# Performance work log

Measured on AMD Instinct MI355X. Metric: run time of the kernel, lower is better.

## Reference

```python
import jax, jax.numpy as jnp
import numpy as np

N_HEAD = 16
MASK_NEG = -10000.0


def setup_inputs() -> dict:
    key = jax.random.key(0)
    k1, k2, k3 = jax.random.split(key, 3)
    B, S, D = 4, 2048, 1024
    x = jax.random.normal(k1, (B, S, D), dtype=jnp.float32)
    c_attn_w = jax.random.normal(k2, (D, 3 * D), dtype=jnp.float32) * 0.02
    c_attn_b = jnp.zeros((3 * D,), dtype=jnp.float32)
    c_proj_w = jax.random.normal(k3, (D, D), dtype=jnp.float32) * 0.02
    c_proj_b = jnp.zeros((D,), dtype=jnp.float32)
    return {"x": x, "c_attn_w": c_attn_w, "c_attn_b": c_attn_b,
            "c_proj_w": c_proj_w, "c_proj_b": c_proj_b}


def reference(x, c_attn_w, c_attn_b, c_proj_w, c_proj_b):
    B, S, D = x.shape
    H = N_HEAD
    Dh = D // H
    # fused QKV projection (Conv1D = x @ W + b)
    qkv = x @ c_attn_w + c_attn_b          # [B,S,3D]
    q, k, v = jnp.split(qkv, 3, axis=-1)   # each [B,S,D]
    # split heads -> [B,H,S,Dh]
    q = q.reshape(B, S, H, Dh).transpose(0, 2, 1, 3)
    k = k.reshape(B, S, H, Dh).transpose(0, 2, 1, 3)
    v = v.reshape(B, S, H, Dh).transpose(0, 2, 1, 3)
    # scores with scaling (scale=True)
    w = jnp.einsum('bhqd,bhkd->bhqk', q, k) / jnp.sqrt(jnp.float32(Dh))
    # multiplicative causal mask: w*b + -10000*(1-b)
    b = jnp.tril(jnp.ones((S, S), dtype=w.dtype))[None, None]  # [1,1,S,S]
    w = w * b + MASK_NEG * (1.0 - b)
    w = jax.nn.softmax(w, axis=-1)
    # dropout is identity at inference
    a = jnp.einsum('bhqk,bhkd->bhqd', w, v)  # [B,H,S,Dh]
    a = a.transpose(0, 2, 1, 3).reshape(B, S, D)  # merge heads
    out = a @ c_proj_w + c_proj_b
    return out
```

## Files before the change

kernel.cpp:

```cpp
#include <hip/hip_runtime.h>

typedef unsigned short u16;
typedef short bf16x8 __attribute__((ext_vector_type(8)));
typedef float f32x4 __attribute__((ext_vector_type(4)));
typedef unsigned int u32;
typedef u32 u32x4 __attribute__((ext_vector_type(4)));

#define B_ 4
#define S_ 2048
#define D_ 1024
#define H_ 16
#define DH_ 64
#define M_ 8192
#define SCL2E 0.1803368801111244f

__device__ __forceinline__ u16 f2b(float f) {
  union { float f; unsigned int u; } v; v.f = f;
  unsigned int u = v.u;
  unsigned int r = (u + 0x7FFFu + ((u >> 16) & 1u)) >> 16;
  return (u16)r;
}

__device__ __forceinline__ void gload16(const void* g, void* l) {
  __builtin_amdgcn_global_load_lds(
      (const __attribute__((address_space(1))) unsigned int*)g,
      (__attribute__((address_space(3))) unsigned int*)l,
      16, 0, 0);
}

__device__ __forceinline__ u32 cvt_pk_bf16(float lo, float hi) {
  u32 r;
  asm("v_cvt_pk_bf16_f32 %0, %1, %2" : "=v"(r) : "v"(lo), "v"(hi));
  return r;
}

struct __attribute__((aligned(8))) u16x4 { u16 x, y, z, w; };

__global__ void cvt_f32_bf16(const float* __restrict__ in, u16* __restrict__ out, int n) {
  int i = (blockIdx.x * blockDim.x + threadIdx.x) * 4;
  if (i >= n) return;
  float4 v = *(const float4*)(in + i);
  u16x4 o; o.x = f2b(v.x); o.y = f2b(v.y); o.z = f2b(v.z); o.w = f2b(v.w);
  *(u16x4*)(out + i) = o;
}

__global__ void transpose_cvt(const float* __restrict__ in, u16* __restrict__ out, int R, int C) {
  __shared__ float tile[32][33];
  int c0 = blockIdx.x * 32, r0 = blockIdx.y * 32;
  int tx = threadIdx.x, ty = threadIdx.y;
#pragma unroll
  for (int j = 0; j < 32; j += 8)
    tile[ty + j][tx] = in[(size_t)(r0 + ty + j) * C + c0 + tx];
  __syncthreads();
#pragma unroll
  for (int j = 0; j < 32; j += 8)
    out[(size_t)(c0 + ty + j) * R + r0 + tx] = f2b(tile[tx][ty + j]);
}

template <int MODE>
__global__ __launch_bounds__(256) void gemm_bt(
    const u16* __restrict__ A, const u16* __restrict__ BT,
    const float* __restrict__ bias, float* __restrict__ outf,
    u16* __restrict__ qb, u16* __restrict__ kb, u16* __restrict__ vtb,
    int Ncols, int Kdim) {
  __shared__ __attribute__((aligned(16))) u16 lsA[2][128 * 64];
  __shared__ __attribute__((aligned(16))) u16 lsB[2][128 * 64];
  const int t = threadIdx.x;
  const int lane = t & 63, w = t >> 6;
  const int lhi = lane >> 4, llo = lane & 15;

  const int gx = gridDim.x;
  const int lin = blockIdx.y * gx + blockIdx.x;
  const int nwg = gx * gridDim.y;
  const int sw = (lin & 7) * (nwg >> 3) + (lin >> 3);
  const int m0 = (sw / gx) * 128, n0 = (sw % gx) * 128;

  const int wr = (w >> 1) * 64, wc = (w & 1) * 64;

  const int r8 = lane >> 3;
  const int scolE = ((lane & 7) ^ r8) * 8;
  const int srow = w * 32 + r8;

  f32x4 acc[4][4] = {};
  const int nt = Kdim >> 6;

#define STAGE_G(buf, kk0)                                                        \
  _Pragma("unroll") for (int j = 0; j < 4; ++j) {                                \
    gload16(A + (size_t)(m0 + srow + j * 8) * Kdim + (kk0) + scolE,              \
            &lsA[buf][(w * 32 + j * 8) * 64]);                                   \
    gload16(BT + (size_t)(n0 + srow + j * 8) * Kdim + (kk0) + scolE,             \
            &lsB[buf][(w * 32 + j * 8) * 64]);                                   \
  }

  STAGE_G(0, 0)
  __syncthreads();

  for (int tt = 0; tt < nt; ++tt) {
    const int cur = tt & 1;
    if (tt + 1 < nt) STAGE_G(cur ^ 1, (tt + 1) << 6)
#pragma unroll
    for (int kk = 0; kk < 2; ++kk) {
      bf16x8 af[4], bfr[4];
#pragma unroll
      for (int i = 0; i < 4; ++i) {
        int ra = wr + i * 16 + llo;
        af[i] = *(const bf16x8*)((const char*)&lsA[cur][ra * 64] +
                                 ((kk * 64 + lhi * 16) ^ ((ra & 7) << 4)));
        int rb = wc + i * 16 + llo;
        bfr[i] = *(const bf16x8*)((const char*)&lsB[cur][rb * 64] +
                                  ((kk * 64 + lhi * 16) ^ ((rb & 7) << 4)));
      }
#pragma unroll
      for (int mi = 0; mi < 4; ++mi)
#pragma unroll
        for (int ni = 0; ni < 4; ++ni)
          acc[mi][ni] = __builtin_amdgcn_mfma_f32_16x16x32_bf16(af[mi], bfr[ni], acc[mi][ni], 0, 0, 0);
    }
    __syncthreads();
  }

  if (MODE == 0) {
#pragma unroll
    for (int mi = 0; mi < 4; ++mi)
#pragma unroll
      for (int ni = 0; ni < 4; ++ni)
#pragma unroll
        for (int r = 0; r < 4; ++r) {
          int m = m0 + wr + mi * 16 + lhi * 4 + r;
          int n = n0 + wc + ni * 16 + llo;
          outf[(size_t)m * Ncols + n] = acc[mi][ni][r] + bias[n];
        }
  } else if (n0 < 1024) {
#pragma unroll
    for (int mi = 0; mi < 4; ++mi)
#pragma unroll
      for (int ni = 0; ni < 4; ++ni)
#pragma unroll
        for (int r = 0; r < 4; ++r) {
          int m = m0 + wr + mi * 16 + lhi * 4 + r;
          int n = n0 + wc + ni * 16 + llo;
          int bidx = m >> 11, s = m & 2047, hh = n >> 6, dh = n & 63;
          qb[((size_t)(bidx * 16 + hh) * 2048 + s) * 64 + dh] =
              f2b((acc[mi][ni][r] + bias[n]) * SCL2E);
        }
  } else if (n0 < 2048) {
#pragma unroll
    for (int mi = 0; mi < 4; ++mi)
#pragma unroll
      for (int ni = 0; ni < 4; ++ni)
#pragma unroll
        for (int r = 0; r < 4; ++r) {
          int m = m0 + wr + mi * 16 + lhi * 4 + r;
          int n2 = n0 - 1024 + wc + ni * 16 + llo;
          int bidx = m >> 11, s = m & 2047, hh = n2 >> 6, dh = n2 & 63;
          kb[((size_t)(bidx * 16 + hh) * 2048 + s) * 64 + dh] =
              f2b(acc[mi][ni][r] + bias[n0 + wc + ni * 16 + llo]);
        }
  } else {
#pragma unroll
    for (int mi = 0; mi < 4; ++mi)
#pragma unroll
      for (int ni = 0; ni < 4; ++ni)
#pragma unroll
        for (int r = 0; r < 4; ++r) {
          int m = m0 + wr + mi * 16 + lhi * 4 + r;
          int n2 = n0 - 2048 + wc + ni * 16 + llo;
          int bidx = m >> 11, s = m & 2047, hh = n2 >> 6, dh = n2 & 63;
          int col = (s & ~127) | ((s & 15) * 8 + ((s >> 4) & 7));
          vtb[((size_t)(bidx * 16 + hh) * 64 + dh) * 2048 + col] =
              f2b(acc[mi][ni][r] + bias[n0 + wc + ni * 16 + llo]);
        }
  }
}

__global__ __launch_bounds__(512) void attn128(
    const u16* __restrict__ Qb, const u16* __restrict__ Kb,
    const u16* __restrict__ VTb, u16* __restrict__ AO) {
  __shared__ __attribute__((aligned(16))) u16 kls[128 * 64];
  __shared__ __attribute__((aligned(16))) u16 vls[64 * 128];
  __shared__ __attribute__((aligned(16))) u16 pl[8][16][136];
  const int t = threadIdx.x, w = t >> 6, lane = t & 63;
  const int lhi = lane >> 4, llo = lane & 15;
  const int bh = blockIdx.y, bb = bh >> 4, hh = bh & 15;
  const u16* Qp = Qb + (size_t)bh * (S_ * DH_);
  const u16* Kp = Kb + (size_t)bh * (S_ * DH_);
  const u16* Vp = VTb + (size_t)bh * (DH_ * S_);
  const int pr = blockIdx.x;

  bf16x8 ones;
#pragma unroll
  for (int i = 0; i < 8; ++i) ones[i] = (short)0x3F80;

  int krow[2], kcolE[2], kdst[2], vrow[2], vcolE[2], vdst[2];
#pragma unroll
  for (int c = 0; c < 2; ++c) {
    int b = c * 8192 + t * 16;
    krow[c] = b >> 7;
    kcolE[c] = (b & 127) >> 1;
    kdst[c] = krow[c] * 128 + ((b & 127) ^ ((krow[c] & 7) << 4));
    vrow[c] = b >> 8;
    vcolE[c] = (b & 255) >> 1;
    vdst[c] = vrow[c] * 256 + ((b & 255) ^ ((vrow[c] & 15) << 4));
  }

  for (int ci = 0; ci < 2; ++ci) {
    const int qc = ci ? (15 - pr) : pr;
    const int q0 = qc * 128;
    const int qrow = q0 + w * 16 + llo;
    bf16x8 aq0 = *(const bf16x8*)(Qp + (size_t)qrow * DH_ + lhi * 8);
    bf16x8 aq1 = *(const bf16x8*)(Qp + (size_t)qrow * DH_ + 32 + lhi * 8);
    const int n128 = qc + 1;

    bf16x8 kst[2], vst[2];
#pragma unroll
    for (int c = 0; c < 2; ++c) {
      kst[c] = *(const bf16x8*)(Kp + (size_t)krow[c] * DH_ + kcolE[c]);
      vst[c] = *(const bf16x8*)(Vp + (size_t)vrow[c] * S_ + vcolE[c]);
    }
    __syncthreads();
#pragma unroll
    for (int c = 0; c < 2; ++c) {
      *(bf16x8*)((char*)kls + kdst[c]) = kst[c];
      *(bf16x8*)((char*)vls + vdst[c]) = vst[c];
    }
    __syncthreads();

    f32x4 o[4] = {};
    f32x4 osum = {};
    const int crow = q0 + w * 16 + lhi * 4;

    for (int tt = 0; tt < n128; ++tt) {
      const int kv0 = tt << 7;
      const bool pf = (tt + 1 < n128);

      f32x4 sc[8] = {};
      const int sw = (llo & 7) << 4;
      __builtin_amdgcn_s_setprio(1);
#pragma unroll
      for (int f = 0; f < 8; ++f) {
        const char* base = (const char*)kls + (f * 16 + llo) * 128;
        bf16x8 bk0 = *(const bf16x8*)(base + ((lhi * 16) ^ sw));
        bf16x8 bk1 = *(const bf16x8*)(base + ((64 + lhi * 16) ^ sw));
        sc[f] = __builtin_amdgcn_mfma_f32_16x16x32_bf16(aq0, bk0, sc[f], 0, 0, 0);
        sc[f] = __builtin_amdgcn_mfma_f32_16x16x32_bf16(aq1, bk1, sc[f], 0, 0, 0);
      }
      __builtin_amdgcn_s_setprio(0);

      if (pf) {
#pragma unroll
        for (int c = 0; c < 2; ++c) {
          kst[c] = *(const bf16x8*)(Kp + (size_t)(kv0 + 128 + krow[c]) * DH_ + kcolE[c]);
          vst[c] = *(const bf16x8*)(Vp + (size_t)vrow[c] * S_ + kv0 + 128 + vcolE[c]);
        }
      }

      const bool lastit = (tt == n128 - 1);
#pragma unroll
      for (int r = 0; r < 4; ++r) {
        float p[8];
#pragma unroll
        for (int f = 0; f < 8; ++f) {
          float x = sc[f][r];
          if (lastit && (kv0 + f * 16 + llo > crow + r)) x = -1e30f;
          p[f] = exp2f(x);
        }
        u32x4 pw;
        pw[0] = cvt_pk_bf16(p[0], p[1]);
        pw[1] = cvt_pk_bf16(p[2], p[3]);
        pw[2] = cvt_pk_bf16(p[4], p[5]);
        pw[3] = cvt_pk_bf16(p[6], p[7]);
        *(u32x4*)((char*)&pl[w][lhi * 4 + r][0] + llo * 16) = pw;
      }

      __builtin_amdgcn_s_setprio(1);
#pragma unroll
      for (int kk = 0; kk < 4; ++kk) {
        bf16x8 ap = *(const bf16x8*)((const char*)&pl[w][llo][0] + kk * 64 + lhi * 16);
#pragma unroll
        for (int f = 0; f < 4; ++f) {
          const char* vbase = (const char*)vls + (f * 16 + llo) * 256;
          bf16x8 bv = *(const bf16x8*)(vbase + ((kk * 64 + lhi * 16) ^ (llo << 4)));
          o[f] = __builtin_amdgcn_mfma_f32_16x16x32_bf16(ap, bv, o[f], 0, 0, 0);
        }
        osum = __builtin_amdgcn_mfma_f32_16x16x32_bf16(ap, ones, osum, 0, 0, 0);
      }
      __builtin_amdgcn_s_setprio(0);

      if (pf) {
        __syncthreads();
#pragma unroll
        for (int c = 0; c < 2; ++c) {
          *(bf16x8*)((char*)kls + kdst[c]) = kst[c];
          *(bf16x8*)((char*)vls + vdst[c]) = vst[c];
        }
        __syncthreads();
      }
    }

#pragma unroll
    for (int f = 0; f < 4; ++f)
#pragma unroll
      for (int r = 0; r < 4; ++r) {
        int row = crow + r;
        int dh = f * 16 + llo;
        float val = o[f][r] / osum[r];
        AO[((size_t)bb * S_ + row) * D_ + hh * DH_ + dh] = f2b(val);
      }
  }
}

extern "C" void kernel_launch(void* const* d_in, const int* in_sizes, int n_in,
                              void* d_out, int out_size, void* d_ws, size_t ws_size,
                              hipStream_t stream) {
  const float* x  = (const float*)d_in[0];
  const float* w1 = (const float*)d_in[1];
  const float* b1 = (const float*)d_in[2];
  const float* w2 = (const float*)d_in[3];
  const float* b2 = (const float*)d_in[4];
  float* out = (float*)d_out;
  char* ws = (char*)d_ws;

  u16* xb  = (u16*)(ws);
  u16* w1t = (u16*)(ws + 16777216);
  u16* w2t = (u16*)(ws + 23068672);
  u16* qb  = (u16*)(ws + 25165824);
  u16* kb  = (u16*)(ws + 41943040);
  u16* vtb = (u16*)(ws + 58720256);
  u16* ao  = xb;

  cvt_f32_bf16<<<8192, 256, 0, stream>>>(x, xb, M_ * D_);
  transpose_cvt<<<dim3(96, 32), dim3(32, 8), 0, stream>>>(w1, w1t, 1024, 3072);
  transpose_cvt<<<dim3(32, 32), dim3(32, 8), 0, stream>>>(w2, w2t, 1024, 1024);

  gemm_bt<1><<<dim3(24, 64), 256, 0, stream>>>(xb, w1t, b1, nullptr, qb, kb, vtb, 3072, 1024);
  attn128<<<dim3(8, 64), 512, 0, stream>>>(qb, kb, vtb, ao);
  gemm_bt<0><<<dim3(8, 64), 256, 0, stream>>>(ao, w2t, b2, out, nullptr, nullptr, nullptr, 1024, 1024);
}
```

Baseline: 188.4 us.

## Restructure GEMM to 256x128 tiles with 8 waves and split-phase load pipelining

The bf16 GEMM kernel moves from 128x128 tiles with 4 waves to 256x128 tiles with 8 waves (512 threads). Each wave computes a 128x32 slab. Global-to-LDS loads for the next K step are issued in pieces between two MFMA phases, with explicit vmcnt waits, s_barrier and s_setprio to raise MFMA priority. The aim is to increase B-tile reuse and overlap memory traffic with compute. In exchange it uses more LDS per block and halves the grid size, which may reduce occupancy and wave-level parallelism.

```diff
diff --git a/kernel.cpp b/kernel.cpp
--- a/kernel.cpp
+++ b/kernel.cpp
@@ -58,12 +58,12 @@
 }
 
 template <int MODE>
-__global__ __launch_bounds__(256) void gemm_bt(
+__global__ __launch_bounds__(512) void gemm_bt(
     const u16* __restrict__ A, const u16* __restrict__ BT,
     const float* __restrict__ bias, float* __restrict__ outf,
     u16* __restrict__ qb, u16* __restrict__ kb, u16* __restrict__ vtb,
     int Ncols, int Kdim) {
-  __shared__ __attribute__((aligned(16))) u16 lsA[2][128 * 64];
+  __shared__ __attribute__((aligned(16))) u16 lsA[2][256 * 64];
   __shared__ __attribute__((aligned(16))) u16 lsB[2][128 * 64];
   const int t = threadIdx.x;
   const int lane = t & 63, w = t >> 6;
@@ -73,102 +73,145 @@
   const int lin = blockIdx.y * gx + blockIdx.x;
   const int nwg = gx * gridDim.y;
   const int sw = (lin & 7) * (nwg >> 3) + (lin >> 3);
-  const int m0 = (sw / gx) * 128, n0 = (sw % gx) * 128;
-
-  const int wr = (w >> 1) * 64, wc = (w & 1) * 64;
+  const int n0 = (sw % gx) * 128, m0 = (sw / gx) * 256;
+
+  const int wr = w >> 2, wc = w & 3;
 
   const int r8 = lane >> 3;
-  const int scolE = ((lane & 7) ^ r8) * 8;
-  const int srow = w * 32 + r8;
-
-  f32x4 acc[4][4] = {};
+  const int scol = ((lane & 7) ^ r8) * 8;
+
+#define ISS_A(buf, kk0, h)                                                        \
+  _Pragma("unroll") for (int j = 0; j < 2; ++j)                                   \
+    gload16(A + (size_t)(m0 + (h) * 128 + w * 16 + j * 8 + r8) * Kdim + (kk0) + scol, \
+            &lsA[buf][(h) * 8192 + w * 1024 + j * 512]);
+#define ISS_B(buf, kk0)                                                           \
+  _Pragma("unroll") for (int j = 0; j < 2; ++j)                                   \
+    gload16(BT + (size_t)(n0 + w * 16 + j * 8 + r8) * Kdim + (kk0) + scol,        \
+            &lsB[buf][w * 1024 + j * 512]);
+
+  f32x4 acc[8][2] = {};
   const int nt = Kdim >> 6;
 
-#define STAGE_G(buf, kk0)                                                        \
-  _Pragma("unroll") for (int j = 0; j < 4; ++j) {                                \
-    gload16(A + (size_t)(m0 + srow + j * 8) * Kdim + (kk0) + scolE,              \
-            &lsA[buf][(w * 32 + j * 8) * 64]);                                   \
-    gload16(BT + (size_t)(n0 + srow + j * 8) * Kdim + (kk0) + scolE,             \
-            &lsB[buf][(w * 32 + j * 8) * 64]);                                   \
+  ISS_A(0, 0, 0)
+  ISS_A(0, 0, 1)
+  ISS_B(0, 0)
+
+  for (int kt = 0; kt < nt; ++kt) {
+    const int cur = kt & 1, nxt = cur ^ 1;
+    const int kn = (kt + 1) << 6;
+    if (kt + 1 < nt) {
+      ISS_A(nxt, kn, 0)
+      asm volatile("s_waitcnt vmcnt(2)" ::: "memory");
+    } else {
+      asm volatile("s_waitcnt vmcnt(0)" ::: "memory");
+    }
+    __builtin_amdgcn_sched_barrier(0);
+    __builtin_amdgcn_s_barrier();
+
+    bf16x8 af[4][2], bfv[2][2];
+#pragma unroll
+    for (int i = 0; i < 4; ++i)
+#pragma unroll
+      for (int kh = 0; kh < 2; ++kh) {
+        int ra = wr * 128 + i * 16 + llo;
+        af[i][kh] = *(const bf16x8*)((const char*)&lsA[cur][0] + ra * 128 +
+                                     ((kh * 64 + lhi * 16) ^ ((ra & 7) << 4)));
+      }
+#pragma unroll
+    for (int pn = 0; pn < 2; ++pn)
+#pragma unroll
+      for (int kh = 0; kh < 2; ++kh) {
+        int rb = wc * 32 + pn * 16 + llo;
+        bfv[pn][kh] = *(const bf16x8*)((const char*)&lsB[cur][0] + rb * 128 +
+                                       ((kh * 64 + lhi * 16) ^ ((rb & 7) << 4)));
+      }
+    if (kt + 1 < nt) { ISS_A(nxt, kn, 1) }
+    __builtin_amdgcn_s_setprio(1);
+#pragma unroll
+    for (int kh = 0; kh < 2; ++kh)
+#pragma unroll
+      for (int i = 0; i < 4; ++i)
+#pragma unroll
+        for (int pn = 0; pn < 2; ++pn)
+          acc[i][pn] = __builtin_amdgcn_mfma_f32_16x16x32_bf16(af[i][kh], bfv[pn][kh], acc[i][pn], 0, 0, 0);
+    __builtin_amdgcn_s_setprio(0);
+    __builtin_amdgcn_s_barrier();
+
+#pragma unroll
+    for (int i = 0; i < 4; ++i)
+#pragma unroll
+      for (int kh = 0; kh < 2; ++kh) {
+        int ra = wr * 128 + 64 + i * 16 + llo;
+        af[i][kh] = *(const bf16x8*)((const char*)&lsA[cur][0] + ra * 128 +
+                                     ((kh * 64 + lhi * 16) ^ ((ra & 7) << 4)));
+      }
+    if (kt + 1 < nt) { ISS_B(nxt, kn) }
+    __builtin_amdgcn_s_setprio(1);
+#pragma unroll
+    for (int kh = 0; kh < 2; ++kh)
+#pragma unroll
+      for (int i = 0; i < 4; ++i)
+#pragma unroll
+        for (int pn = 0; pn < 2; ++pn)
+          acc[4 + i][pn] = __builtin_amdgcn_mfma_f32_16x16x32_bf16(af[i][kh], bfv[pn][kh], acc[4 + i][pn], 0, 0, 0);
+    __builtin_amdgcn_s_setprio(0);
+    __builtin_amdgcn_s_barrier();
   }
-
-  STAGE_G(0, 0)
-  __syncthreads();
-
-  for (int tt = 0; tt < nt; ++tt) {
-    const int cur = tt & 1;
-    if (tt + 1 < nt) STAGE_G(cur ^ 1, (tt + 1) << 6)
-#pragma unroll
-    for (int kk = 0; kk < 2; ++kk) {
-      bf16x8 af[4], bfr[4];
-#pragma unroll
-      for (int i = 0; i < 4; ++i) {
-        int ra = wr + i * 16 + llo;
-        af[i] = *(const bf16x8*)((const char*)&lsA[cur][ra * 64] +
-                                 ((kk * 64 + lhi * 16) ^ ((ra & 7) << 4)));
-        int rb = wc + i * 16 + llo;
-        bfr[i] = *(const bf16x8*)((const char*)&lsB[cur][rb * 64] +
-                                  ((kk * 64 + lhi * 16) ^ ((rb & 7) << 4)));
-      }
-#pragma unroll
-      for (int mi = 0; mi < 4; ++mi)
-#pragma unroll
-        for (int ni = 0; ni < 4; ++ni)
-          acc[mi][ni] = __builtin_amdgcn_mfma_f32_16x16x32_bf16(af[mi], bfr[ni], acc[mi][ni], 0, 0, 0);
-    }
-    __syncthreads();
-  }
+#undef ISS_A
+#undef ISS_B
 
   if (MODE == 0) {
 #pragma unroll
-    for (int mi = 0; mi < 4; ++mi)
-#pragma unroll
-      for (int ni = 0; ni < 4; ++ni)
+    for (int mi = 0; mi < 8; ++mi)
+#pragma unroll
+      for (int ni = 0; ni < 2; ++ni)
 #pragma unroll
         for (int r = 0; r < 4; ++r) {
-          int m = m0 + wr + mi * 16 + lhi * 4 + r;
-          int n = n0 + wc + ni * 16 + llo;
+          int m = m0 + wr * 128 + mi * 16 + lhi * 4 + r;
+          int n = n0 + wc * 32 + ni * 16 + llo;
           outf[(size_t)m * Ncols + n] = acc[mi][ni][r] + bias[n];
         }
   } else if (n0 < 1024) {
 #pragma unroll
-    for (int mi = 0; mi < 4; ++mi)
-#pragma unroll
-      for (int ni = 0; ni < 4; ++ni)
+    for (int mi = 0; mi < 8; ++mi)
+#pragma unroll
+      for (int ni = 0; ni < 2; ++ni)
 #pragma unroll
         for (int r = 0; r < 4; ++r) {
-          int m = m0 + wr + mi * 16 + lhi * 4 + r;
-          int n = n0 + wc + ni * 16 + llo;
+          int m = m0 + wr * 128 + mi * 16 + lhi * 4 + r;
+          int n = n0 + wc * 32 + ni * 16 + llo;
           int bidx = m >> 11, s = m & 2047, hh = n >> 6, dh = n & 63;
           qb[((size_t)(bidx * 16 + hh) * 2048 + s) * 64 + dh] =
               f2b((acc[mi][ni][r] + bias[n]) * SCL2E);
         }
   } else if (n0 < 2048) {
 #pragma unroll
-    for (int mi = 0; mi < 4; ++mi)
-#pragma unroll
-      for (int ni = 0; ni < 4; ++ni)
+    for (int mi = 0; mi < 8; ++mi)
+#pragma unroll
+      for (int ni = 0; ni < 2; ++ni)
 #pragma unroll
         for (int r = 0; r < 4; ++r) {
-          int m = m0 + wr + mi * 16 + lhi * 4 + r;
-          int n2 = n0 - 1024 + wc + ni * 16 + llo;
+          int m = m0 + wr * 128 + mi * 16 + lhi * 4 + r;
+          int n = n0 + wc * 32 + ni * 16 + llo;
+          int n2 = n - 1024;
           int bidx = m >> 11, s = m & 2047, hh = n2 >> 6, dh = n2 & 63;
           kb[((size_t)(bidx * 16 + hh) * 2048 + s) * 64 + dh] =
-              f2b(acc[mi][ni][r] + bias[n0 + wc + ni * 16 + llo]);
+              f2b(acc[mi][ni][r] + bias[n]);
         }
   } else {
 #pragma unroll
-    for (int mi = 0; mi < 4; ++mi)
-#pragma unroll
-      for (int ni = 0; ni < 4; ++ni)
+    for (int mi = 0; mi < 8; ++mi)
+#pragma unroll
+      for (int ni = 0; ni < 2; ++ni)
 #pragma unroll
         for (int r = 0; r < 4; ++r) {
-          int m = m0 + wr + mi * 16 + lhi * 4 + r;
-          int n2 = n0 - 2048 + wc + ni * 16 + llo;
+          int m = m0 + wr * 128 + mi * 16 + lhi * 4 + r;
+          int n = n0 + wc * 32 + ni * 16 + llo;
+          int n2 = n - 2048;
           int bidx = m >> 11, s = m & 2047, hh = n2 >> 6, dh = n2 & 63;
           int col = (s & ~127) | ((s & 15) * 8 + ((s >> 4) & 7));
           vtb[((size_t)(bidx * 16 + hh) * 64 + dh) * 2048 + col] =
-              f2b(acc[mi][ni][r] + bias[n0 + wc + ni * 16 + llo]);
+              f2b(acc[mi][ni][r] + bias[n]);
         }
   }
 }
@@ -332,7 +375,7 @@
   transpose_cvt<<<dim3(96, 32), dim3(32, 8), 0, stream>>>(w1, w1t, 1024, 3072);
   transpose_cvt<<<dim3(32, 32), dim3(32, 8), 0, stream>>>(w2, w2t, 1024, 1024);
 
-  gemm_bt<1><<<dim3(24, 64), 256, 0, stream>>>(xb, w1t, b1, nullptr, qb, kb, vtb, 3072, 1024);
+  gemm_bt<1><<<dim3(24, 32), 512, 0, stream>>>(xb, w1t, b1, nullptr, qb, kb, vtb, 3072, 1024);
   attn128<<<dim3(8, 64), 512, 0, stream>>>(qb, kb, vtb, ao);
-  gemm_bt<0><<<dim3(8, 64), 256, 0, stream>>>(ao, w2t, b2, out, nullptr, nullptr, nullptr, 1024, 1024);
-}
+  gemm_bt<0><<<dim3(8, 32), 512, 0, stream>>>(ao, w2t, b2, out, nullptr, nullptr, nullptr, 1024, 1024);
+}
```

Result: slower. 215.9 us (+14.6%).

## Enlarge attention query tile to 256 rows per block for K/V reuse

Applied to the files above, without the earlier changes.

The attention kernel now processes 256 query rows per block (two 16-row sub-tiles per wave) instead of 128, so each staged 128-row K/V tile in LDS is reused by twice as many queries. This halves global K/V traffic and the barriers per query. The grid shrinks to 4x64 blocks (256 blocks), which may under-fill the GPU's compute units and raises register pressure from the doubled accumulators. The causal mask is applied on the last two KV tiles.

```diff
diff --git a/kernel.cpp b/kernel.cpp
--- a/kernel.cpp
+++ b/kernel.cpp
@@ -118,6 +118,7 @@
     }
     __syncthreads();
   }
+#undef STAGE_G
 
   if (MODE == 0) {
 #pragma unroll
@@ -173,7 +174,7 @@
   }
 }
 
-__global__ __launch_bounds__(512) void attn128(
+__global__ __launch_bounds__(512) void attn256(
     const u16* __restrict__ Qb, const u16* __restrict__ Kb,
     const u16* __restrict__ VTb, u16* __restrict__ AO) {
   __shared__ __attribute__((aligned(16))) u16 kls[128 * 64];
@@ -204,12 +205,17 @@
   }
 
   for (int ci = 0; ci < 2; ++ci) {
-    const int qc = ci ? (15 - pr) : pr;
-    const int q0 = qc * 128;
-    const int qrow = q0 + w * 16 + llo;
-    bf16x8 aq0 = *(const bf16x8*)(Qp + (size_t)qrow * DH_ + lhi * 8);
-    bf16x8 aq1 = *(const bf16x8*)(Qp + (size_t)qrow * DH_ + 32 + lhi * 8);
-    const int n128 = qc + 1;
+    const int qc = ci ? (7 - pr) : pr;
+    const int q0 = qc * 256;
+    const int n128 = 2 * qc + 2;
+
+    bf16x8 aq[2][2];
+#pragma unroll
+    for (int s = 0; s < 2; ++s) {
+      const int qrow = q0 + w * 32 + s * 16 + llo;
+      aq[s][0] = *(const bf16x8*)(Qp + (size_t)qrow * DH_ + lhi * 8);
+      aq[s][1] = *(const bf16x8*)(Qp + (size_t)qrow * DH_ + 32 + lhi * 8);
+    }
 
     bf16x8 kst[2], vst[2];
 #pragma unroll
@@ -225,66 +231,69 @@
     }
     __syncthreads();
 
-    f32x4 o[4] = {};
-    f32x4 osum = {};
-    const int crow = q0 + w * 16 + lhi * 4;
+    f32x4 o[2][4] = {};
+    f32x4 osum[2] = {};
 
     for (int tt = 0; tt < n128; ++tt) {
       const int kv0 = tt << 7;
       const bool pf = (tt + 1 < n128);
-
-      f32x4 sc[8] = {};
-      const int sw = (llo & 7) << 4;
-      __builtin_amdgcn_s_setprio(1);
-#pragma unroll
-      for (int f = 0; f < 8; ++f) {
-        const char* base = (const char*)kls + (f * 16 + llo) * 128;
-        bf16x8 bk0 = *(const bf16x8*)(base + ((lhi * 16) ^ sw));
-        bf16x8 bk1 = *(const bf16x8*)(base + ((64 + lhi * 16) ^ sw));
-        sc[f] = __builtin_amdgcn_mfma_f32_16x16x32_bf16(aq0, bk0, sc[f], 0, 0, 0);
-        sc[f] = __builtin_amdgcn_mfma_f32_16x16x32_bf16(aq1, bk1, sc[f], 0, 0, 0);
+      const bool masked = (tt >= n128 - 2);
+      const int swz = (llo & 7) << 4;
+
+#pragma unroll
+      for (int s = 0; s < 2; ++s) {
+        f32x4 sc[8] = {};
+        __builtin_amdgcn_s_setprio(1);
+#pragma unroll
+        for (int f = 0; f < 8; ++f) {
+          const char* base = (const char*)kls + (f * 16 + llo) * 128;
+          bf16x8 bk0 = *(const bf16x8*)(base + ((lhi * 16) ^ swz));
+          bf16x8 bk1 = *(const bf16x8*)(base + ((64 + lhi * 16) ^ swz));
+          sc[f] = __builtin_amdgcn_mfma_f32_16x16x32_bf16(aq[s][0], bk0, sc[f], 0, 0, 0);
+          sc[f] = __builtin_amdgcn_mfma_f32_16x16x32_bf16(aq[s][1], bk1, sc[f], 0, 0, 0);
+        }
+        __builtin_amdgcn_s_setprio(0);
+
+        if (s == 0 && pf) {
+#pragma unroll
+          for (int c = 0; c < 2; ++c) {
+            kst[c] = *(const bf16x8*)(Kp + (size_t)(kv0 + 128 + krow[c]) * DH_ + kcolE[c]);
+            vst[c] = *(const bf16x8*)(Vp + (size_t)vrow[c] * S_ + kv0 + 128 + vcolE[c]);
+          }
+        }
+
+        const int crow = q0 + w * 32 + s * 16 + lhi * 4;
+#pragma unroll
+        for (int r = 0; r < 4; ++r) {
+          float p[8];
+#pragma unroll
+          for (int f = 0; f < 8; ++f) {
+            float x = sc[f][r];
+            if (masked && (kv0 + f * 16 + llo > crow + r)) x = -1e30f;
+            p[f] = exp2f(x);
+          }
+          u32x4 pw;
+          pw[0] = cvt_pk_bf16(p[0], p[1]);
+          pw[1] = cvt_pk_bf16(p[2], p[3]);
+          pw[2] = cvt_pk_bf16(p[4], p[5]);
+          pw[3] = cvt_pk_bf16(p[6], p[7]);
+          *(u32x4*)((char*)&pl[w][lhi * 4 + r][0] + llo * 16) = pw;
+        }
+
+        __builtin_amdgcn_s_setprio(1);
+#pragma unroll
+        for (int kk = 0; kk < 4; ++kk) {
+          bf16x8 ap = *(const bf16x8*)((const char*)&pl[w][llo][0] + kk * 64 + lhi * 16);
+#pragma unroll
+          for (int f = 0; f < 4; ++f) {
+            const char* vbase = (const char*)vls + (f * 16 + llo) * 256;
+            bf16x8 bv = *(const bf16x8*)(vbase + ((kk * 64 + lhi * 16) ^ (llo << 4)));
+            o[s][f] = __builtin_amdgcn_mfma_f32_16x16x32_bf16(ap, bv, o[s][f], 0, 0, 0);
+          }
+          osum[s] = __builtin_amdgcn_mfma_f32_16x16x32_bf16(ap, ones, osum[s], 0, 0, 0);
+        }
+        __builtin_amdgcn_s_setprio(0);
       }
-      __builtin_amdgcn_s_setprio(0);
-
-      if (pf) {
-#pragma unroll
-        for (int c = 0; c < 2; ++c) {
-          kst[c] = *(const bf16x8*)(Kp + (size_t)(kv0 + 128 + krow[c]) * DH_ + kcolE[c]);
-          vst[c] = *(const bf16x8*)(Vp + (size_t)vrow[c] * S_ + kv0 + 128 + vcolE[c]);
-        }
-      }
-
-      const bool lastit = (tt == n128 - 1);
-#pragma unroll
-      for (int r = 0; r < 4; ++r) {
-        float p[8];
-#pragma unroll
-        for (int f = 0; f < 8; ++f) {
-          float x = sc[f][r];
-          if (lastit && (kv0 + f * 16 + llo > crow + r)) x = -1e30f;
-          p[f] = exp2f(x);
-        }
-        u32x4 pw;
-        pw[0] = cvt_pk_bf16(p[0], p[1]);
-        pw[1] = cvt_pk_bf16(p[2], p[3]);
-        pw[2] = cvt_pk_bf16(p[4], p[5]);
-        pw[3] = cvt_pk_bf16(p[6], p[7]);
-        *(u32x4*)((char*)&pl[w][lhi * 4 + r][0] + llo * 16) = pw;
-      }
-
-      __builtin_amdgcn_s_setprio(1);
-#pragma unroll
-      for (int kk = 0; kk < 4; ++kk) {
-        bf16x8 ap = *(const bf16x8*)((const char*)&pl[w][llo][0] + kk * 64 + lhi * 16);
-#pragma unroll
-        for (int f = 0; f < 4; ++f) {
-          const char* vbase = (const char*)vls + (f * 16 + llo) * 256;
-          bf16x8 bv = *(const bf16x8*)(vbase + ((kk * 64 + lhi * 16) ^ (llo << 4)));
-          o[f] = __builtin_amdgcn_mfma_f32_16x16x32_bf16(ap, bv, o[f], 0, 0, 0);
-        }
-        osum = __builtin_amdgcn_mfma_f32_16x16x32_bf16(ap, ones, osum, 0, 0, 0);
-      }
-      __builtin_amdgcn_s_setprio(0);
 
       if (pf) {
         __syncthreads();
@@ -298,14 +307,16 @@
     }
 
 #pragma unroll
-    for (int f = 0; f < 4; ++f)
-#pragma unroll
-      for (int r = 0; r < 4; ++r) {
-        int row = crow + r;
-        int dh = f * 16 + llo;
-        float val = o[f][r] / osum[r];
-        AO[((size_t)bb * S_ + row) * D_ + hh * DH_ + dh] = f2b(val);
-      }
+    for (int s = 0; s < 2; ++s)
+#pragma unroll
+      for (int f = 0; f < 4; ++f)
+#pragma unroll
+        for (int r = 0; r < 4; ++r) {
+          int row = q0 + w * 32 + s * 16 + lhi * 4 + r;
+          int dh = f * 16 + llo;
+          float val = o[s][f][r] / osum[s][r];
+          AO[((size_t)bb * S_ + row) * D_ + hh * DH_ + dh] = f2b(val);
+        }
   }
 }
 
@@ -333,6 +344,6 @@
   transpose_cvt<<<dim3(32, 32), dim3(32, 8), 0, stream>>>(w2, w2t, 1024, 1024);
 
   gemm_bt<1><<<dim3(24, 64), 256, 0, stream>>>(xb, w1t, b1, nullptr, qb, kb, vtb, 3072, 1024);
-  attn128<<<dim3(8, 64), 512, 0, stream>>>(qb, kb, vtb, ao);
+  attn256<<<dim3(4, 64), 512, 0, stream>>>(qb, kb, vtb, ao);
   gemm_bt<0><<<dim3(8, 64), 256, 0, stream>>>(ao, w2t, b2, out, nullptr, nullptr, nullptr, 1024, 1024);
 }
```

New measurement: 197.2 us. 1.05x slower.
